# Optimization experiments

Hardware: AMD Instinct MI355X
Metric: run time of the kernel (lower is better)

Reference implementation:

```python
import jax, jax.numpy as jnp
import numpy as np

WS = 4      # window_size (RSUT5 default)
SHIFT = 2   # window_size // 2
NH = 8      # num_heads
DIM = 256
H0 = W0 = T0 = 32
B0 = 1


def _ln(x, g, b, eps=1e-5):
    m = x.mean(-1, keepdims=True)
    v = ((x - m) ** 2).mean(-1, keepdims=True)
    return (x - m) / jnp.sqrt(v + eps) * g + b


def _rel_index(ws):
    c = np.stack(np.meshgrid(np.arange(ws), np.arange(ws), np.arange(ws), indexing='ij')).reshape(3, -1)
    r = (c[:, :, None] - c[:, None, :]).transpose(1, 2, 0) + (ws - 1)
    return jnp.asarray((r[..., 0] * (2 * ws - 1) + r[..., 1]) * (2 * ws - 1) + r[..., 2])


def _partition(x, ws):
    B, H, W, T, C = x.shape
    x = x.reshape(B, H // ws, ws, W // ws, ws, T // ws, ws, C)
    return x.transpose(0, 1, 3, 5, 2, 4, 6, 7).reshape(-1, ws ** 3, C)


def _reverse(w, ws, B, H, W, T):
    C = w.shape[-1]
    x = w.reshape(B, H // ws, W // ws, T // ws, ws, ws, ws, C)
    return x.transpose(0, 1, 4, 2, 5, 3, 6, 7).reshape(B, H, W, T, C)


def _attn_mask(H, W, T, ws, ss):
    # static (numpy) replica of Block.createmask; H,W,T divisible by ws here
    img = np.zeros((H, W, T), np.float32)
    sls = (slice(0, -ws), slice(-ws, -ss), slice(-ss, None))
    cnt = 0
    for h in sls:
        for w in sls:
            for t in sls:
                img[h, w, t] = cnt
                cnt += 1
    mw = img.reshape(H // ws, ws, W // ws, ws, T // ws, ws).transpose(0, 2, 4, 1, 3, 5).reshape(-1, ws ** 3)
    d = mw[:, None, :] - mw[:, :, None]
    return jnp.asarray(np.where(d != 0, -100.0, 0.0).astype(np.float32))


def _swin(x, H, W, T, shift, mask, n1g, n1b, qkvw, qkvb, rpb, projw, projb, n2g, n2b, fc1w, fc1b, fc2w, fc2b):
    B, L, C = x.shape
    N = WS ** 3
    hd = C // NH
    shortcut = x
    x = _ln(x, n1g, n1b).reshape(B, H, W, T, C)
    if shift:
        x = jnp.roll(x, (-shift, -shift, -shift), axis=(1, 2, 3))
    xw = _partition(x, WS)                                        # [B*nW, N, C]
    qkv = (xw @ qkvw.T + qkvb).reshape(-1, N, 3, NH, hd).transpose(2, 0, 3, 1, 4)
    q, k, v = qkv[0], qkv[1], qkv[2]                              # [B*nW, NH, N, hd]
    attn = jnp.einsum('bhnd,bhmd->bhnm', q * (hd ** -0.5), k)
    attn = attn + rpb[_rel_index(WS)].transpose(2, 0, 1)[None]    # relative position bias
    if mask is not None:
        nW = mask.shape[0]
        attn = (attn.reshape(B, nW, NH, N, N) + mask[None, :, None]).reshape(-1, NH, N, N)
    attn = jax.nn.softmax(attn, axis=-1)
    out = jnp.einsum('bhnm,bhmd->bhnd', attn, v).transpose(0, 2, 1, 3).reshape(-1, N, C)
    out = out @ projw.T + projb
    x = _reverse(out, WS, B, H, W, T)
    if shift:
        x = jnp.roll(x, (shift, shift, shift), axis=(1, 2, 3))
    x = shortcut + x.reshape(B, L, C)
    h = _ln(x, n2g, n2b)
    h = jax.nn.gelu(h @ fc1w.T + fc1b, approximate=False) @ fc2w.T + fc2b
    return x + h


def setup_inputs() -> dict:
    key = jax.random.key(0)
    ks = iter(jax.random.split(key, 16))
    def rn(shape, s=0.02):
        return jax.random.normal(next(ks), shape, jnp.float32) * s
    d = {'x': jax.random.normal(next(ks), (B0, H0 * W0 * T0, DIM), jnp.float32),
         'H': H0, 'W': W0, 'T': T0,
         'norm_g': jnp.ones((DIM,), jnp.float32), 'norm_b': jnp.zeros((DIM,), jnp.float32)}
    for p in ('w', 's'):
        d[p + 'n1g'] = jnp.ones((DIM,), jnp.float32); d[p + 'n1b'] = jnp.zeros((DIM,), jnp.float32)
        d[p + 'qkvw'] = rn((3 * DIM, DIM)); d[p + 'qkvb'] = jnp.zeros((3 * DIM,), jnp.float32)
        d[p + 'rpb'] = rn(((2 * WS - 1) ** 3, NH))
        d[p + 'projw'] = rn((DIM, DIM)); d[p + 'projb'] = jnp.zeros((DIM,), jnp.float32)
        d[p + 'n2g'] = jnp.ones((DIM,), jnp.float32); d[p + 'n2b'] = jnp.zeros((DIM,), jnp.float32)
        d[p + 'fc1w'] = rn((4 * DIM, DIM)); d[p + 'fc1b'] = jnp.zeros((4 * DIM,), jnp.float32)
        d[p + 'fc2w'] = rn((DIM, 4 * DIM)); d[p + 'fc2b'] = jnp.zeros((DIM,), jnp.float32)
    return d


def reference(x, H, W, T, norm_g, norm_b,
              wn1g, wn1b, wqkvw, wqkvb, wrpb, wprojw, wprojb, wn2g, wn2b, wfc1w, wfc1b, wfc2w, wfc2b,
              sn1g, sn1b, sqkvw, sqkvb, srpb, sprojw, sprojb, sn2g, sn2b, sfc1w, sfc1b, sfc2w, sfc2b):
    mask = _attn_mask(H, W, T, WS, SHIFT)
    x = _swin(x, H, W, T, 0, None, wn1g, wn1b, wqkvw, wqkvb, wrpb, wprojw, wprojb, wn2g, wn2b, wfc1w, wfc1b, wfc2w, wfc2b)
    x = _swin(x, H, W, T, SHIFT, mask, sn1g, sn1b, sqkvw, sqkvb, srpb, sprojw, sprojb, sn2g, sn2b, sfc1w, sfc1b, sfc2w, sfc2b)
    B, L, C = x.shape
    # Block.norm + toConv: [B, L, C] -> [B, C, H, W, T]
    return _ln(x, norm_g, norm_b).reshape(B, H, W, T, C).transpose(0, 4, 1, 2, 3)
```

## Files before the change

### kernel.cpp

```cpp
#include <hip/hip_runtime.h>

typedef unsigned short u16;
typedef unsigned int   u32;
typedef __bf16 bfx8 __attribute__((ext_vector_type(8)));
typedef float  fx4  __attribute__((ext_vector_type(4)));

__device__ __forceinline__ u16 f2b(float f) {
    union { float f; u32 i; } v; v.f = f;
    u32 r = (v.i + 0x7fffu + ((v.i >> 16) & 1u)) >> 16;
    return (u16)r;
}
__device__ __forceinline__ u32 pk(float a, float b) {
    return (u32)f2b(a) | ((u32)f2b(b) << 16);
}

__device__ __forceinline__ void gl2lds16(const u16* g, u16* l) {
    __builtin_amdgcn_global_load_lds(
        (const __attribute__((address_space(1))) u32*)(const void*)g,
        (__attribute__((address_space(3))) u32*)(void*)l, 16, 0, 0);
}

__device__ __forceinline__ int map_token(int r, int shift) {
    int win = r >> 6, n = r & 63;
    int wh = win >> 6, ww = (win >> 3) & 7, wt = win & 7;
    int h = wh * 4 + (n >> 4);
    int w = ww * 4 + ((n >> 2) & 3);
    int t = wt * 4 + (n & 3);
    h = (h + shift) & 31; w = (w + shift) & 31; t = (t + shift) & 31;
    return (h << 10) | (w << 5) | t;
}

__device__ __forceinline__ float gelu_fast(float v) {
    float t = v * v;
    float u = v * __builtin_fmaf(t, 0.044715f, 1.0f);
    float e = __expf(-1.5957691216057308f * u);
    return v * __builtin_amdgcn_rcpf(1.0f + e);
}

struct CvtArgs { const float* src[8]; int cum[9]; };
__global__ __launch_bounds__(256) void cvt_kernel(CvtArgs a, u16* __restrict__ dst) {
    int g = (blockIdx.x * 256 + threadIdx.x) * 4;
    int t = 0;
    #pragma unroll
    for (int i = 1; i < 8; i++) t += (g >= a.cum[i]);
    int local = g - a.cum[t];
    float4 f = *(const float4*)(a.src[t] + local);
    uint2 o; o.x = pk(f.x, f.y); o.y = pk(f.z, f.w);
    *(uint2*)(dst + g) = o;
}

template<int GATHER, int F32OUT>
__global__ __launch_bounds__(256) void ln_kernel(const float* __restrict__ resid,
                                                 const float* __restrict__ g, const float* __restrict__ b,
                                                 void* __restrict__ outp, int shift) {
    int lane = threadIdx.x & 63;
    int row  = blockIdx.x * 4 + (threadIdx.x >> 6);
    int src  = GATHER ? map_token(row, shift) : row;
    float4 x = ((const float4*)(resid + src * 256))[lane];
    float s1 = x.x + x.y + x.z + x.w;
    float s2 = x.x * x.x + x.y * x.y + x.z * x.z + x.w * x.w;
    #pragma unroll
    for (int off = 1; off < 64; off <<= 1) { s1 += __shfl_xor(s1, off); s2 += __shfl_xor(s2, off); }
    float mean = s1 * (1.0f / 256.0f);
    float var  = s2 * (1.0f / 256.0f) - mean * mean;
    float rstd = rsqrtf(var + 1e-5f);
    int c = lane * 4;
    float4 gv = *(const float4*)(g + c);
    float4 bv = *(const float4*)(b + c);
    float y0 = (x.x - mean) * rstd * gv.x + bv.x;
    float y1 = (x.y - mean) * rstd * gv.y + bv.y;
    float y2 = (x.z - mean) * rstd * gv.z + bv.z;
    float y3 = (x.w - mean) * rstd * gv.w + bv.w;
    if (F32OUT) {
        float4 o; o.x = y0; o.y = y1; o.z = y2; o.w = y3;
        *(float4*)((float*)outp + row * 256 + c) = o;
    } else {
        uint2 o; o.x = pk(y0, y1); o.y = pk(y2, y3);
        *(uint2*)((u16*)outp + row * 256 + c) = o;
    }
}

template<int EPI>
__global__ __launch_bounds__(256) void gemm2(const u16* __restrict__ A, const u16* __restrict__ W,
                                             const float* __restrict__ bias,
                                             u16* __restrict__ outb, float* __restrict__ resid,
                                             int Nout, int K, int shift,
                                             const float* __restrict__ rsrc) {
    __shared__ u16 As[2][128 * 32];
    __shared__ u16 Bs[2][128 * 32];
    int lane = threadIdx.x & 63, w = threadIdx.x >> 6;
    int wm = w >> 1, wn = w & 1;
    int m0 = blockIdx.x * 128, n0 = blockIdx.y * 128;
    int lr = lane & 15, q = lane >> 4;
    int sw = q ^ ((lr >> 1) & 3);

    fx4 acc[4][4] = {};

    auto stage = [&](int kt, int b) {
        #pragma unroll
        for (int p = 0; p < 2; p++) {
            int row = p * 64 + w * 16 + (lane >> 2);
            int kg  = (lane & 3) ^ ((row >> 1) & 3);
            int slot = (p * 256 + w * 64 + lane) * 8;
            gl2lds16(A + (size_t)(m0 + row) * K + kt + kg * 8, &As[b][slot]);
            gl2lds16(W + (size_t)(n0 + row) * K + kt + kg * 8, &Bs[b][slot]);
        }
    };

    stage(0, 0);
    int nk = K >> 5;
    for (int ki = 0; ki < nk; ki++) {
        __syncthreads();
        if (ki + 1 < nk) stage((ki + 1) << 5, (ki + 1) & 1);
        int b = ki & 1;
        bfx8 af[4], bfr[4];
        #pragma unroll
        for (int t = 0; t < 4; t++) {
            int ra = wm * 64 + t * 16 + lr;
            int rb = wn * 64 + t * 16 + lr;
            af[t]  = *(const bfx8*)(&As[b][(ra * 4 + sw) * 8]);
            bfr[t] = *(const bfx8*)(&Bs[b][(rb * 4 + sw) * 8]);
        }
        #pragma unroll
        for (int i = 0; i < 4; i++)
            #pragma unroll
            for (int j = 0; j < 4; j++)
                acc[i][j] = __builtin_amdgcn_mfma_f32_16x16x32_bf16(af[i], bfr[j], acc[i][j], 0, 0, 0);
    }

    float bv[4];
    #pragma unroll
    for (int j = 0; j < 4; j++) bv[j] = bias[n0 + wn * 64 + j * 16 + lr];
    #pragma unroll
    for (int i = 0; i < 4; i++) {
        #pragma unroll
        for (int r = 0; r < 4; r++) {
            int gr = m0 + wm * 64 + i * 16 + q * 4 + r;
            int orow = (EPI == 3) ? map_token(gr, shift) : gr;
            #pragma unroll
            for (int j = 0; j < 4; j++) {
                int gc = n0 + wn * 64 + j * 16 + lr;
                float v = acc[i][j][r] + bv[j];
                if (EPI == 0) {
                    outb[(size_t)gr * Nout + gc] = f2b(v);
                } else if (EPI == 1) {
                    outb[(size_t)gr * Nout + gc] = f2b(gelu_fast(v));
                } else {
                    resid[orow * 256 + gc] = rsrc[orow * 256 + gc] + v;
                }
            }
        }
    }
}

__global__ __launch_bounds__(128) void attn_mfma(const u16* __restrict__ qkv, const float* __restrict__ rpb,
                                                 u16* __restrict__ outb, int masked) {
    __shared__ u16  Pl[2][64][72];
    __shared__ u16  VT[2][32][72];
    __shared__ float rbS[2][344];
    int w = threadIdx.x >> 6;
    int lane = threadIdx.x & 63;
    int id = blockIdx.x * 2 + w;
    int win = id >> 3, head = id & 7;
    int lr = lane & 15, q = lane >> 4;

    const u16* base = qkv + (size_t)win * 64 * 768 + head * 32;

    bfx8 qf[4], kf[4];
    #pragma unroll
    for (int t = 0; t < 4; t++) {
        const u16* rq = base + (lr + 16 * t) * 768 + q * 8;
        qf[t] = *(const bfx8*)(rq);
        kf[t] = *(const bfx8*)(rq + 256);
    }
    {
        const u16* rv = base + lane * 768 + 512;
        #pragma unroll
        for (int c = 0; c < 32; c += 8) {
            bfx8 vv = *(const bfx8*)(rv + c);
            #pragma unroll
            for (int j = 0; j < 8; j++) VT[w][c + j][lane] = ((const u16*)&vv)[j];
        }
    }
    for (int i = lane; i < 343; i += 64) rbS[w][i] = rpb[i * 8 + head];

    fx4 sT[4][4] = {};
    #pragma unroll
    for (int jt = 0; jt < 4; jt++)
        #pragma unroll
        for (int it = 0; it < 4; it++)
            sT[jt][it] = __builtin_amdgcn_mfma_f32_16x16x32_bf16(kf[jt], qf[it], sT[jt][it], 0, 0, 0);

    int wh = win >> 6, ww = (win >> 3) & 7, wt = win & 7;
    const float scale = 0.17677669529663687f;

    #pragma unroll
    for (int it = 0; it < 4; it++) {
        int i = lr + 16 * it;
        int ih = i >> 4, iw = (i >> 2) & 3, iT = i & 3;
        int labn = 0;
        if (masked) {
            int lh = (wh == 7) ? (1 + (ih >> 1)) : 0;
            int lw = (ww == 7) ? (1 + (iw >> 1)) : 0;
            int lt = (wt == 7) ? (1 + (iT >> 1)) : 0;
            labn = lh * 9 + lw * 3 + lt;
        }
        float sv[4][4];
        float mx = -1e30f;
        #pragma unroll
        for (int jt = 0; jt < 4; jt++)
            #pragma unroll
            for (int r = 0; r < 4; r++) {
                int j = q * 4 + r + 16 * jt;
                int jh = j >> 4, jw = (j >> 2) & 3, jT = j & 3;
                float s = sT[jt][it][r] * scale +
                          rbS[w][((ih - jh + 3) * 7 + (iw - jw + 3)) * 7 + (iT - jT + 3)];
                if (masked) {
                    int lh = (wh == 7) ? (1 + (jh >> 1)) : 0;
                    int lw = (ww == 7) ? (1 + (jw >> 1)) : 0;
                    int lt = (wt == 7) ? (1 + (jT >> 1)) : 0;
                    if (lh * 9 + lw * 3 + lt != labn) s -= 100.0f;
                }
                sv[jt][r] = s;
                mx = fmaxf(mx, s);
            }
        mx = fmaxf(mx, __shfl_xor(mx, 16));
        mx = fmaxf(mx, __shfl_xor(mx, 32));
        float sum = 0.f;
        #pragma unroll
        for (int jt = 0; jt < 4; jt++)
            #pragma unroll
            for (int r = 0; r < 4; r++) { sv[jt][r] = __expf(sv[jt][r] - mx); sum += sv[jt][r]; }
        sum += __shfl_xor(sum, 16);
        sum += __shfl_xor(sum, 32);
        float inv = 1.0f / sum;
        #pragma unroll
        for (int jt = 0; jt < 4; jt++) {
            uint2 pw;
            pw.x = pk(sv[jt][0] * inv, sv[jt][1] * inv);
            pw.y = pk(sv[jt][2] * inv, sv[jt][3] * inv);
            *(uint2*)&Pl[w][i][q * 4 + 16 * jt] = pw;
        }
    }

    fx4 o[4][2] = {};
    #pragma unroll
    for (int kk = 0; kk < 2; kk++) {
        bfx8 pf[4], vf[2];
        #pragma unroll
        for (int it = 0; it < 4; it++) pf[it] = *(const bfx8*)&Pl[w][lr + 16 * it][q * 8 + 32 * kk];
        #pragma unroll
        for (int dt = 0; dt < 2; dt++) vf[dt] = *(const bfx8*)&VT[w][lr + 16 * dt][q * 8 + 32 * kk];
        #pragma unroll
        for (int it = 0; it < 4; it++)
            #pragma unroll
            for (int dt = 0; dt < 2; dt++)
                o[it][dt] = __builtin_amdgcn_mfma_f32_16x16x32_bf16(pf[it], vf[dt], o[it][dt], 0, 0, 0);
    }

    u16* ob = outb + (size_t)win * 64 * 256 + head * 32;
    #pragma unroll
    for (int it = 0; it < 4; it++)
        #pragma unroll
        for (int r = 0; r < 4; r++) {
            int i = 16 * it + q * 4 + r;
            #pragma unroll
            for (int dt = 0; dt < 2; dt++)
                ob[i * 256 + 16 * dt + lr] = f2b(o[it][dt][r]);
        }
}

__global__ __launch_bounds__(256) void ln_tr(const float* __restrict__ in,
                                             const float* __restrict__ g, const float* __restrict__ b,
                                             float* __restrict__ out) {
    __shared__ float tile[256 * 33];
    int tid = threadIdx.x;
    int r   = tid >> 3;
    int cg  = (tid & 7) * 32;
    int row = blockIdx.x * 32 + r;
    const float* src = in + (size_t)row * 256 + cg;

    float v[32];
    float s1 = 0.f, s2 = 0.f;
    #pragma unroll
    for (int j = 0; j < 8; j++) {
        float4 f = *(const float4*)(src + 4 * j);
        v[4*j] = f.x; v[4*j+1] = f.y; v[4*j+2] = f.z; v[4*j+3] = f.w;
        s1 += f.x + f.y + f.z + f.w;
        s2 += f.x*f.x + f.y*f.y + f.z*f.z + f.w*f.w;
    }
    #pragma unroll
    for (int off = 1; off < 8; off <<= 1) { s1 += __shfl_xor(s1, off); s2 += __shfl_xor(s2, off); }
    float mean = s1 * (1.0f / 256.0f);
    float rstd = rsqrtf(s2 * (1.0f / 256.0f) - mean * mean + 1e-5f);

    #pragma unroll
    for (int j = 0; j < 8; j++) {
        float4 gv = *(const float4*)(g + cg + 4 * j);
        float4 bv = *(const float4*)(b + cg + 4 * j);
        int c0 = cg + 4 * j;
        int slot = (r + (c0 >> 2)) & 31;
        tile[(c0 + 0) * 33 + slot] = (v[4*j]   - mean) * rstd * gv.x + bv.x;
        tile[(c0 + 1) * 33 + slot] = (v[4*j+1] - mean) * rstd * gv.y + bv.y;
        tile[(c0 + 2) * 33 + slot] = (v[4*j+2] - mean) * rstd * gv.z + bv.z;
        tile[(c0 + 3) * 33 + slot] = (v[4*j+3] - mean) * rstd * gv.w + bv.w;
    }
    __syncthreads();

    int c = tid;
    int csh = (c >> 2) & 31;
    const float* base = &tile[c * 33];
    float o[32];
    #pragma unroll
    for (int r2 = 0; r2 < 32; r2++) o[r2] = base[(r2 + csh) & 31];

    float* dst = out + (size_t)c * 32768 + blockIdx.x * 32;
    #pragma unroll
    for (int j = 0; j < 8; j++) {
        float4 f; f.x = o[4*j]; f.y = o[4*j+1]; f.z = o[4*j+2]; f.w = o[4*j+3];
        *(float4*)(dst + 4 * j) = f;
    }
}

extern "C" void kernel_launch(void* const* d_in, const int* in_sizes, int n_in,
                              void* d_out, int out_size, void* d_ws, size_t ws_size,
                              hipStream_t stream) {
    const float* x      = (const float*)d_in[0];
    const float* norm_g = (const float*)d_in[4];
    const float* norm_b = (const float*)d_in[5];

    char* wsb = (char*)d_ws;
    float* resid = (float*)wsb;
    u16*   xn    = (u16*)(wsb + (size_t)32 * 1024 * 1024);
    u16*   big   = (u16*)(wsb + (size_t)48 * 1024 * 1024);
    u16*   attnb = (u16*)(wsb + (size_t)96 * 1024 * 1024);
    u16*   wb    = (u16*)(wsb + (size_t)112 * 1024 * 1024);

    CvtArgs ca;
    static const int offs[9] = {0, 196608, 262144, 524288, 786432, 983040, 1048576, 1310720, 1572864};
    for (int i = 0; i < 9; i++) ca.cum[i] = offs[i];
    ca.src[0] = (const float*)d_in[6 + 2];
    ca.src[1] = (const float*)d_in[6 + 5];
    ca.src[2] = (const float*)d_in[6 + 9];
    ca.src[3] = (const float*)d_in[6 + 11];
    ca.src[4] = (const float*)d_in[19 + 2];
    ca.src[5] = (const float*)d_in[19 + 5];
    ca.src[6] = (const float*)d_in[19 + 9];
    ca.src[7] = (const float*)d_in[19 + 11];
    cvt_kernel<<<1536, 256, 0, stream>>>(ca, wb);

    for (int blk = 0; blk < 2; blk++) {
        void* const* P = d_in + 6 + blk * 13;
        const float* n1g  = (const float*)P[0];
        const float* n1b  = (const float*)P[1];
        const float* qkvb = (const float*)P[3];
        const float* rpb  = (const float*)P[4];
        const float* pjb  = (const float*)P[6];
        const float* n2g  = (const float*)P[7];
        const float* n2b  = (const float*)P[8];
        const float* f1b  = (const float*)P[10];
        const float* f2b_ = (const float*)P[12];
        const u16* qkvw = wb + offs[0] + blk * 786432;
        const u16* pjw  = wb + offs[1] + blk * 786432;
        const u16* f1w  = wb + offs[2] + blk * 786432;
        const u16* f2w  = wb + offs[3] + blk * 786432;
        int shift = blk ? 2 : 0;

        const float* ln1src = blk ? resid : x;
        const float* projadd = blk ? resid : x;

        ln_kernel<1, 0><<<8192, 256, 0, stream>>>(ln1src, n1g, n1b, xn, shift);
        gemm2<0><<<dim3(256, 6), 256, 0, stream>>>(xn, qkvw, qkvb, big, nullptr, 768, 256, 0, nullptr);
        attn_mfma<<<2048, 128, 0, stream>>>(big, rpb, attnb, blk);
        gemm2<3><<<dim3(256, 2), 256, 0, stream>>>(attnb, pjw, pjb, nullptr, resid, 256, 256, shift, projadd);
        ln_kernel<0, 0><<<8192, 256, 0, stream>>>(resid, n2g, n2b, xn, 0);
        gemm2<1><<<dim3(256, 8), 256, 0, stream>>>(xn, f1w, f1b, big, nullptr, 1024, 256, 0, nullptr);
        gemm2<2><<<dim3(256, 2), 256, 0, stream>>>(big, f2w, f2b_, nullptr, resid, 256, 1024, 0, resid);
    }

    ln_tr<<<1024, 256, 0, stream>>>(resid, norm_g, norm_b, (float*)d_out);
}
```

Before: 467.1 us.

## Triple-buffer GEMM LDS staging with explicit vmcnt waits and hoisted addressing

The GEMM main loop moves from double to triple buffering of the A/B tiles in LDS, prefetching two K-steps ahead. A partial s_waitcnt vmcnt replaces the implicit full wait before each barrier, so loads for the next stage can stay in flight during compute. Global pointers, swizzled slots and LDS read offsets are precomputed outside the loop to cut per-iteration address arithmetic. LDS use rises by half, which may lower occupancy. The hand-written waitcnt and barrier ordering depend on the assumed count of outstanding loads.

```diff
diff --git a/kernel.cpp b/kernel.cpp
--- a/kernel.cpp
+++ b/kernel.cpp
@@ -86,46 +86,61 @@
                                              u16* __restrict__ outb, float* __restrict__ resid,
                                              int Nout, int K, int shift,
                                              const float* __restrict__ rsrc) {
-    __shared__ u16 As[2][128 * 32];
-    __shared__ u16 Bs[2][128 * 32];
+    __shared__ u16 As[3][4096];
+    __shared__ u16 Bs[3][4096];
     int lane = threadIdx.x & 63, w = threadIdx.x >> 6;
     int wm = w >> 1, wn = w & 1;
     int m0 = blockIdx.x * 128, n0 = blockIdx.y * 128;
     int lr = lane & 15, q = lane >> 4;
     int sw = q ^ ((lr >> 1) & 3);
 
+    int rowS  = w * 16 + (lane >> 2);
+    int kg    = (lane & 3) ^ ((rowS >> 1) & 3);
+    int slot0 = (w * 64 + lane) * 8;
+    int slot1 = slot0 + 2048;
+    const u16* gA0 = A + (size_t)(m0 + rowS) * K + kg * 8;
+    const u16* gA1 = A + (size_t)(m0 + rowS + 64) * K + kg * 8;
+    const u16* gB0 = W + (size_t)(n0 + rowS) * K + kg * 8;
+    const u16* gB1 = W + (size_t)(n0 + rowS + 64) * K + kg * 8;
+
+    int oA[4], oB[4];
+    #pragma unroll
+    for (int t = 0; t < 4; t++) {
+        oA[t] = ((wm * 64 + t * 16 + lr) * 4 + sw) * 8;
+        oB[t] = ((wn * 64 + t * 16 + lr) * 4 + sw) * 8;
+    }
+
     fx4 acc[4][4] = {};
 
     auto stage = [&](int kt, int b) {
-        #pragma unroll
-        for (int p = 0; p < 2; p++) {
-            int row = p * 64 + w * 16 + (lane >> 2);
-            int kg  = (lane & 3) ^ ((row >> 1) & 3);
-            int slot = (p * 256 + w * 64 + lane) * 8;
-            gl2lds16(A + (size_t)(m0 + row) * K + kt + kg * 8, &As[b][slot]);
-            gl2lds16(W + (size_t)(n0 + row) * K + kt + kg * 8, &Bs[b][slot]);
-        }
+        gl2lds16(gA0 + kt, &As[b][slot0]);
+        gl2lds16(gA1 + kt, &As[b][slot1]);
+        gl2lds16(gB0 + kt, &Bs[b][slot0]);
+        gl2lds16(gB1 + kt, &Bs[b][slot1]);
     };
 
+    int nk = K >> 5;
     stage(0, 0);
-    int nk = K >> 5;
+    if (nk > 1) stage(32, 1);
+    int b0 = 0, b1 = 1, b2 = 2;
     for (int ki = 0; ki < nk; ki++) {
-        __syncthreads();
-        if (ki + 1 < nk) stage((ki + 1) << 5, (ki + 1) & 1);
-        int b = ki & 1;
+        if (ki + 1 < nk) asm volatile("s_waitcnt vmcnt(4)" ::: "memory");
+        else             asm volatile("s_waitcnt vmcnt(0)" ::: "memory");
+        __builtin_amdgcn_s_barrier();
+        __builtin_amdgcn_sched_barrier(0);
+        if (ki + 2 < nk) stage((ki + 2) << 5, b2);
         bfx8 af[4], bfr[4];
         #pragma unroll
         for (int t = 0; t < 4; t++) {
-            int ra = wm * 64 + t * 16 + lr;
-            int rb = wn * 64 + t * 16 + lr;
-            af[t]  = *(const bfx8*)(&As[b][(ra * 4 + sw) * 8]);
-            bfr[t] = *(const bfx8*)(&Bs[b][(rb * 4 + sw) * 8]);
+            af[t]  = *(const bfx8*)(&As[b0][oA[t]]);
+            bfr[t] = *(const bfx8*)(&Bs[b0][oB[t]]);
         }
         #pragma unroll
         for (int i = 0; i < 4; i++)
             #pragma unroll
             for (int j = 0; j < 4; j++)
                 acc[i][j] = __builtin_amdgcn_mfma_f32_16x16x32_bf16(af[i], bfr[j], acc[i][j], 0, 0, 0);
+        int tmp = b0; b0 = b1; b1 = b2; b2 = tmp;
     }
 
     float bv[4];
```

New measurement: 467.4 us. About the same (+0.1%).
